# Kernel optimization log

Measured on AMD Instinct MI355X. Metric: run time of the kernel, lower is better.

## Reference

```python
import jax, jax.numpy as jnp
import numpy as np

TGT, BSZ, E, H, HD, P = 256, 64, 1024, 16, 64, 16
TAU = 3.0  # gumbel temperature
SCALE = 1.0 / np.sqrt(HD)


def setup_inputs() -> dict:
    rng = jax.random.key(0)
    ks = jax.random.split(rng, 14)
    n = lambda i, s: jax.random.normal(ks[i], s, dtype=jnp.float32)
    u = jax.random.uniform(ks[7], (BSZ, 2), dtype=jnp.float32, minval=1e-6, maxval=1.0 - 1e-6)
    return {
        'idx': 0,
        'query': n(0, (TGT, BSZ, E)),
        'key': n(1, (TGT, BSZ, E)),
        'value': n(2, (TGT, BSZ, E)),
        'prefix': n(3, (BSZ, 2, P, E)) * 0.5,  # gathered prefix_pool[prompt_ids]
        'batch_weight': jax.random.uniform(ks[4], (BSZ,), dtype=jnp.float32),
        'ori_image_features': n(5, (BSZ, 512)),
        'gumbel_noise': -jnp.log(-jnp.log(u)),  # standard gumbel(0,1) noise
        'in_proj_w': n(8, (3 * E, E)) * 0.02,
        'in_proj_b': jnp.zeros((3 * E,), jnp.float32),
        'out_w': n(9, (E, E)) * 0.02,
        'out_b': jnp.zeros((E,), jnp.float32),
        'gumbel_w': n(10, (2, 512)) * 0.05,
        'gumbel_b': jnp.zeros((2,), jnp.float32),
    }


def _sdpa(q, k, v):
    # q:[b,h,t,d] k,v:[b,h,s,d]
    s = jnp.einsum('bhtd,bhsd->bhts', q, k) * SCALE
    a = jax.nn.softmax(s, axis=-1)
    return jnp.einsum('bhts,bhsd->bhtd', a, v)


def reference(idx, query, key, value, prefix, batch_weight, ori_image_features,
              gumbel_noise, in_proj_w, in_proj_b, out_w, out_b, gumbel_w, gumbel_b):
    tgt, bsz, e = query.shape
    src = key.shape[0]
    # packed in-projection (w chunked into q/k/v blocks)
    w_q, w_k, w_v = jnp.split(in_proj_w, 3, axis=0)
    b_q, b_k, b_v = jnp.split(in_proj_b, 3, axis=0)
    q = query @ w_q.T + b_q            # [t,b,E]
    k = key @ w_k.T + b_k              # [s,b,E]
    v = value @ w_v.T + b_v
    # -> [b,h,t,d]
    q = q.reshape(tgt, bsz, H, HD).transpose(1, 2, 0, 3)
    k = k.reshape(src, bsz, H, HD).transpose(1, 2, 0, 3)
    v = v.reshape(src, bsz, H, HD).transpose(1, 2, 0, 3)
    # prefix k/v: [b,P,E] -> [b,h,P,d] (no in-projection, used raw as in source)
    pk = prefix[:, 0].reshape(bsz, P, H, HD).transpose(0, 2, 1, 3)
    pv = prefix[:, 1].reshape(bsz, P, H, HD).transpose(0, 2, 1, 3)

    attn = _sdpa(q, k, v)                      # [b,h,t,d]
    attn_flat = attn.transpose(2, 0, 1, 3).reshape(tgt * bsz, e)  # (t,b) row order

    attn_pre = _sdpa(q, pk, pv) * batch_weight[:, None, None, None]
    attn_pre_flat = attn_pre.transpose(2, 0, 1, 3).reshape(tgt * bsz, e)

    # gumbel-softmax gate (soft), one 2-way gate per sample
    logits = ori_image_features @ gumbel_w.T + gumbel_b           # [b,2]
    gumbel = jax.nn.softmax((logits + gumbel_noise) / TAU, axis=-1)
    gate = jnp.repeat(gumbel, tgt, axis=0)                        # [b*t,2] (b,t) order, as in source
    combined = attn_flat * gate[:, :1] + (attn_flat + attn_pre_flat) * gate[:, 1:2]

    out = combined @ out_w.T + out_b
    return out.reshape(tgt, bsz, e)
```

## Files before the change

### kernel.cpp

```cpp
#include <hip/hip_runtime.h>

typedef __attribute__((ext_vector_type(8))) short bf16x8;
typedef __attribute__((ext_vector_type(4))) float f32x4;
typedef __attribute__((ext_vector_type(8))) unsigned short ushort8;
typedef __attribute__((ext_vector_type(4))) unsigned short ushort4v;
typedef __attribute__((ext_vector_type(4))) float float4v;
typedef __attribute__((ext_vector_type(2))) unsigned int uint2v;
typedef __attribute__((ext_vector_type(4))) unsigned int uint4v;

#define TGT 256
#define BSZ 64
#define EMB 1024
#define NH 16
#define HD 64
#define PP 16

__device__ __forceinline__ float b2f(unsigned short u) {
  return __builtin_bit_cast(float, ((unsigned int)u) << 16);
}
__device__ __forceinline__ unsigned short f2b(float f) {
  unsigned int u = __builtin_bit_cast(unsigned int, f);
  u += 0x7fffu + ((u >> 16) & 1u);
  return (unsigned short)(u >> 16);
}
__device__ __forceinline__ unsigned int pack2(float lo, float hi) {
  return (unsigned int)f2b(lo) | ((unsigned int)f2b(hi) << 16);
}
__device__ __forceinline__ f32x4 mfma16(bf16x8 a, bf16x8 b, f32x4 c) {
  return __builtin_amdgcn_mfma_f32_16x16x32_bf16(a, b, c, 0, 0, 0);
}
__device__ __forceinline__ void gl_lds16(const unsigned short* g, unsigned short* l) {
  __builtin_amdgcn_global_load_lds(
      (const __attribute__((address_space(1))) unsigned int*)g,
      (__attribute__((address_space(3))) unsigned int*)l, 16, 0, 0);
}

__global__ __launch_bounds__(64) void gate_kernel(
    const float* __restrict__ feat, const float* __restrict__ gw,
    const float* __restrict__ gb, const float* __restrict__ noise,
    float* __restrict__ g1) {
  const int b = blockIdx.x, lane = threadIdx.x;
  float a0 = 0.f, a1 = 0.f;
  for (int i = lane; i < 512; i += 64) {
    float f = feat[b * 512 + i];
    a0 += f * gw[i];
    a1 += f * gw[512 + i];
  }
#pragma unroll
  for (int off = 32; off >= 1; off >>= 1) {
    a0 += __shfl_xor(a0, off);
    a1 += __shfl_xor(a1, off);
  }
  if (lane == 0) {
    float l0 = (a0 + gb[0] + noise[b * 2 + 0]) * (1.0f / 3.0f);
    float l1 = (a1 + gb[1] + noise[b * 2 + 1]) * (1.0f / 3.0f);
    float mm = fmaxf(l0, l1);
    float e0 = __expf(l0 - mm), e1 = __expf(l1 - mm);
    g1[b] = e1 / (e0 + e1);
  }
}

__global__ __launch_bounds__(256) void cast_bf16_kernel(
    const float* __restrict__ in, unsigned short* __restrict__ out, int n8) {
  int i = blockIdx.x * blockDim.x + threadIdx.x;
  const int stride = gridDim.x * blockDim.x;
  for (; i < n8; i += stride) {
    const float4v* p = (const float4v*)(in + (size_t)i * 8);
    float4v v0 = p[0], v1 = p[1];
    ushort8 o = {f2b(v0[0]), f2b(v0[1]), f2b(v0[2]), f2b(v0[3]),
                 f2b(v1[0]), f2b(v1[1]), f2b(v1[2]), f2b(v1[3])};
    *(ushort8*)(out + (size_t)i * 8) = o;
  }
}

#define STEP_WAIT(cntstr)                                \
  asm volatile("s_waitcnt " cntstr ::: "memory");        \
  __builtin_amdgcn_sched_barrier(0);                     \
  __builtin_amdgcn_s_barrier();

#define P3_ISSUE(t, P)                                   \
  {                                                      \
    const float* _p = a32p + (size_t)(t) * 32;           \
    ar[P][0] = *(const float4v*)_p;                      \
    ar[P][1] = *(const float4v*)(_p + 4);                \
    ar[P][2] = *(const float4v*)(_p + 131072);           \
    ar[P][3] = *(const float4v*)(_p + 131072 + 4);       \
  }
#define P3_WRITE(P)                                                     \
  {                                                                     \
    float4v* v = ar[P];                                                 \
    uint4v h0 = {pack2(v[0][0], v[0][1]), pack2(v[0][2], v[0][3]),      \
                 pack2(v[1][0], v[1][1]), pack2(v[1][2], v[1][3])};     \
    uint4v h1 = {pack2(v[2][0], v[2][1]), pack2(v[2][2], v[2][3]),      \
                 pack2(v[3][0], v[3][1]), pack2(v[3][2], v[3][3])};     \
    unsigned short* d = &As[P][swA];                                    \
    *(uint4v*)d = h0;                                                   \
    *(uint4v*)(d + 4096) = h1;                                          \
  }
#define B_STAGE_SLOT(s, SL)                              \
  {                                                      \
    int k0s = (s) * 32;                                  \
    unsigned short* d = &Bs[SL][wl];                     \
    gl_lds16(b0p + k0s, d);                              \
    gl_lds16(b1p + k0s, d + 4096);                       \
  }
#define P3_STEP(s, PAR, BS, DO_IA, DO_SB, DO_W)                       \
  {                                                                   \
    const unsigned short* Ab = &As[PAR][0];                           \
    const unsigned short* Bb = &Bs[BS][0];                            \
    bf16x8 af[8], bfr[4];                                             \
    _Pragma("unroll") for (int mi = 0; mi < 8; ++mi)                  \
        af[mi] = *(const bf16x8*)&Ab[aoff + mi * 512];                \
    _Pragma("unroll") for (int ni = 0; ni < 4; ++ni)                  \
        bfr[ni] = *(const bf16x8*)&Bb[boff + ni * 512];               \
    if (DO_IA) P3_ISSUE((s) + 2, PAR);                                \
    if (DO_SB) B_STAGE_SLOT((s) + 3, ((BS) + 3) & 3);                 \
    __builtin_amdgcn_s_setprio(1);                                    \
    _Pragma("unroll") for (int mi = 0; mi < 8; ++mi)                  \
      _Pragma("unroll") for (int ni = 0; ni < 4; ++ni)                \
        acc[mi][ni] = mfma16(af[mi], bfr[ni], acc[mi][ni]);           \
    __builtin_amdgcn_s_setprio(0);                                    \
    if (DO_W) P3_WRITE((PAR) ^ 1);                 \
  }

__global__ __launch_bounds__(512, 2) void proj3_kernel(
    const float* __restrict__ q, const float* __restrict__ kk,
    const float* __restrict__ vv, const unsigned short* __restrict__ W3,
    const float* __restrict__ bias3, unsigned short* __restrict__ C3) {
  constexpr int K = 1024;
  __shared__ __attribute__((aligned(16))) unsigned short As[2][8192];
  __shared__ __attribute__((aligned(16))) unsigned short Bs[4][8192];
  const int pj = blockIdx.y;
  const float* A = (pj == 0) ? q : ((pj == 1) ? kk : vv);
  const unsigned short* W = W3 + (size_t)pj * 1024 * 1024;
  const float* bias = bias3 + pj * 1024;
  unsigned short* Cv = C3 + (size_t)pj * 16384 * 1024;
  const float qsc = (pj == 0) ? 0.125f : 1.0f;

  const int tid = threadIdx.x;
  const int wv = tid >> 6, lane = tid & 63;
  const int l15 = lane & 15, kg = lane >> 4;
  const int bid = blockIdx.x;
  const int cpx = gridDim.x >> 3;
  const int wg = (bid & 7) * cpx + (bid >> 3);
  const int m0 = (wg >> 2) * 256, n0 = (wg & 3) * 256;
  const int wmL = (wv >> 2) * 128, wnL = (wv & 3) * 64;

  const int sr = wv * 16 + (lane >> 2);
  const int sc = ((lane & 3) * 8) ^ (((sr >> 1) & 3) << 3);
  const float* a32p = A + (size_t)(m0 + sr) * K + (lane & 3) * 8;
  const int swA = sr * 32 + (((lane & 3) ^ ((sr >> 1) & 3)) << 3);
  float4v ar[2][4];
  const unsigned short* b0p = W + (size_t)(n0 + sr) * K + sc;
  const unsigned short* b1p = b0p + (size_t)128 * K;
  const int wl = wv * 512;

  const int x = ((l15 >> 1) & 3) << 3;
  const int aoff = (wmL + l15) * 32 + ((kg * 8) ^ x);
  const int boff = (wnL + l15) * 32 + ((kg * 8) ^ x);

  f32x4 acc[8][4];
#pragma unroll
  for (int i = 0; i < 8; ++i)
#pragma unroll
    for (int j = 0; j < 4; ++j) acc[i][j] = (f32x4){0.f, 0.f, 0.f, 0.f};

  P3_ISSUE(0, 0); B_STAGE_SLOT(0, 0); P3_ISSUE(1, 1); B_STAGE_SLOT(1, 1);
  B_STAGE_SLOT(2, 2);
  P3_WRITE(0);
  STEP_WAIT("vmcnt(8) lgkmcnt(0)")

#pragma unroll 1
  for (int sb = 0; sb < 28; sb += 4) {
    P3_STEP(sb + 0, 0, 0, 1, 1, 1);
    STEP_WAIT("vmcnt(8) lgkmcnt(0)")
    P3_STEP(sb + 1, 1, 1, 1, 1, 1);
    STEP_WAIT("vmcnt(8) lgkmcnt(0)")
    P3_STEP(sb + 2, 0, 2, 1, 1, 1);
    STEP_WAIT("vmcnt(8) lgkmcnt(0)")
    P3_STEP(sb + 3, 1, 3, 1, 1, 1);
    STEP_WAIT("vmcnt(8) lgkmcnt(0)")
  }
  P3_STEP(28, 0, 0, 1, 1, 1);
  STEP_WAIT("vmcnt(8) lgkmcnt(0)")
  P3_STEP(29, 1, 1, 1, 0, 1);
  STEP_WAIT("vmcnt(8) lgkmcnt(0)")
  P3_STEP(30, 0, 2, 0, 0, 1);
  STEP_WAIT("vmcnt(0) lgkmcnt(0)")
  P3_STEP(31, 1, 3, 0, 0, 0);

#pragma unroll
  for (int mi = 0; mi < 8; ++mi) {
#pragma unroll
    for (int ni = 0; ni < 4; ++ni) {
      int col = n0 + wnL + ni * 16 + l15;
      float bcol = bias[col];
#pragma unroll
      for (int r = 0; r < 4; ++r) {
        int row = m0 + wmL + mi * 16 + kg * 4 + r;
        float v = (acc[mi][ni][r] + bcol) * qsc;
        int t = row >> 6, bb = row & 63, hh = col >> 6, dd = col & 63;
        Cv[(size_t)((bb * 16 + hh) * 256 + t) * 64 + dd] = f2b(v);
      }
    }
  }
}

#define O_AOFF(s) (((s) >> 1) * 16384 + ((s)&1) * 32)
#define O_STAGE_A(s)                                     \
  {                                                      \
    const unsigned short* _ap = abf + O_AOFF(s);         \
    unsigned short* d = &As[(s) & 3][wl];                \
    gl_lds16(_ap, d);                                    \
    gl_lds16(_ap + 128, d + 4096);                       \
  }
#define O_STAGE_B(s)                                     \
  {                                                      \
    int k0s = (s) * 32;                                  \
    unsigned short* d = &Bs[(s) & 3][wl];                \
    gl_lds16(b0p + k0s, d);                              \
    gl_lds16(b1p + k0s, d + 4096);                       \
  }
#define O_STEP(s, DO_STAGE)                                           \
  {                                                                   \
    const unsigned short* Ab = &As[(s) & 3][0];                       \
    const unsigned short* Bb = &Bs[(s) & 3][0];                       \
    bf16x8 af[8], bfr[4];                                             \
    _Pragma("unroll") for (int mi = 0; mi < 8; ++mi)                  \
        af[mi] = *(const bf16x8*)&Ab[aoff + mi * 512];                \
    _Pragma("unroll") for (int ni = 0; ni < 4; ++ni)                  \
        bfr[ni] = *(const bf16x8*)&Bb[boff + ni * 512];               \
    if (DO_STAGE) {                                                   \
      O_STAGE_A((s) + 3);                                             \
      O_STAGE_B((s) + 3);                                             \
    }                                                                 \
    __builtin_amdgcn_s_setprio(1);                                    \
    _Pragma("unroll") for (int mi = 0; mi < 8; ++mi)                  \
      _Pragma("unroll") for (int ni = 0; ni < 4; ++ni)                \
        acc[mi][ni] = mfma16(af[mi], bfr[ni], acc[mi][ni]);           \
    __builtin_amdgcn_s_setprio(0);                                    \
  }

__global__ __launch_bounds__(512, 2) void gemm256o_kernel(
    const unsigned short* __restrict__ A, const unsigned short* __restrict__ W,
    const float* __restrict__ bias, float* __restrict__ Cv) {
  constexpr int K = 1024, N = 1024;
  __shared__ __attribute__((aligned(16))) unsigned short As[4][8192];
  __shared__ __attribute__((aligned(16))) unsigned short Bs[4][8192];
  const int tid = threadIdx.x;
  const int wv = tid >> 6, lane = tid & 63;
  const int l15 = lane & 15, kg = lane >> 4;
  const int bid = blockIdx.x;
  const int cpx = gridDim.x >> 3;
  const int wg = (bid & 7) * cpx + (bid >> 3);
  const int m0 = (wg >> 2) * 256, n0 = (wg & 3) * 256;
  const int wmL = (wv >> 2) * 128, wnL = (wv & 3) * 64;

  const int sr = wv * 16 + (lane >> 2);
  const int sc = ((lane & 3) * 8) ^ (((sr >> 1) & 3) << 3);
  const int srg = m0 + sr;
  const unsigned short* abf =
      A + (size_t)(srg & 63) * 262144 + (srg >> 6) * 64 + sc;
  const unsigned short* b0p = W + (size_t)(n0 + sr) * K + sc;
  const unsigned short* b1p = b0p + (size_t)128 * K;
  const int wl = wv * 512;

  const int x = ((l15 >> 1) & 3) << 3;
  const int aoff = (wmL + l15) * 32 + ((kg * 8) ^ x);
  const int boff = (wnL + l15) * 32 + ((kg * 8) ^ x);

  f32x4 acc[8][4];
#pragma unroll
  for (int i = 0; i < 8; ++i)
#pragma unroll
    for (int j = 0; j < 4; ++j) acc[i][j] = (f32x4){0.f, 0.f, 0.f, 0.f};

  O_STAGE_A(0); O_STAGE_B(0); O_STAGE_A(1); O_STAGE_B(1); O_STAGE_A(2); O_STAGE_B(2);
  STEP_WAIT("vmcnt(8)")

  for (int s = 0; s < 29; ++s) {
    O_STEP(s, 1);
    STEP_WAIT("vmcnt(8)")
  }
  O_STEP(29, 0);
  STEP_WAIT("vmcnt(4)")
  O_STEP(30, 0);
  STEP_WAIT("vmcnt(0)")
  O_STEP(31, 0);

#pragma unroll
  for (int mi = 0; mi < 8; ++mi) {
#pragma unroll
    for (int ni = 0; ni < 4; ++ni) {
      int col = n0 + wnL + ni * 16 + l15;
      float bcol = bias[col];
#pragma unroll
      for (int r = 0; r < 4; ++r) {
        int row = m0 + wmL + mi * 16 + kg * 4 + r;
        Cv[(size_t)row * N + col] = acc[mi][ni][r] + bcol;
      }
    }
  }
}

__global__ __launch_bounds__(512) void attn_kernel(
    const unsigned short* __restrict__ qb, const unsigned short* __restrict__ kb,
    const unsigned short* __restrict__ vb, const float* __restrict__ prefix,
    const float* __restrict__ bw, const float* __restrict__ g1,
    unsigned short* __restrict__ comb) {
  const int b = blockIdx.x, h = blockIdx.y;
  __shared__ __attribute__((aligned(16))) unsigned short Kl[256][64];
  __shared__ __attribute__((aligned(16))) unsigned short Vt[64 * 256];
  __shared__ __attribute__((aligned(16))) unsigned short PKl[16][64];
  __shared__ __attribute__((aligned(16))) unsigned short PVt[64][32];
  __shared__ __attribute__((aligned(16))) unsigned short Plds[8][16][40];
  unsigned short* Cb = &Kl[0][0];
  const int tid = threadIdx.x;
  const int wv = tid >> 6, lane = tid & 63;
  const size_t slab = (size_t)(b * NH + h) * 16384;

#pragma unroll
  for (int it = 0; it < 4; ++it) {
    int cid = tid + it * 512;
    int j = cid >> 3, c = cid & 7;
    gl_lds16(kb + slab + (size_t)j * 64 + ((c ^ (j & 7)) << 3),
             &Kl[0][0] + (size_t)(it * 512 + wv * 64) * 8);
    ushort8 vv = *(const ushort8*)(vb + slab + (size_t)j * 64 + (c << 3));
#pragma unroll
    for (int i = 0; i < 8; ++i) {
      int gran = (j >> 3) ^ i ^ c;
      Vt[(c * 8 + i) * 256 + gran * 8 + (j & 7)] = vv[i];
    }
  }
  if (tid < 256) {
    int arr = tid >> 7, cid = tid & 127;
    int sp = cid >> 3, c = cid & 7;
    const float* src = prefix + ((size_t)(b * 2 + arr) * PP + sp) * EMB + h * HD + c * 8;
    float4v v0 = *(const float4v*)src;
    float4v v1 = *(const float4v*)(src + 4);
    if (arr == 0) {
      ushort8 o = {f2b(v0[0]), f2b(v0[1]), f2b(v0[2]), f2b(v0[3]),
                   f2b(v1[0]), f2b(v1[1]), f2b(v1[2]), f2b(v1[3])};
      *(ushort8*)&PKl[sp][((c ^ (sp & 7)) << 3)] = o;
    } else {
#pragma unroll
      for (int i = 0; i < 8; ++i)
        PVt[c * 8 + i][sp] = f2b(i < 4 ? v0[i] : v1[i - 4]);
    }
  } else if (tid < 384) {
    int cid = tid - 256;
    *(ushort8*)&PVt[cid >> 1][16 + (cid & 1) * 8] = (ushort8){0, 0, 0, 0, 0, 0, 0, 0};
  }
  __syncthreads();

  const int l15 = lane & 15, g = lane >> 4;
  const int swl = l15 & 7;
  const float bwb = bw[b];
  unsigned short(&Pw)[16][40] = Plds[wv];

  const int t0 = wv * 32 + l15;
  const size_t qbase = slab + (size_t)t0 * 64;
  bf16x8 qf[2][2];
  qf[0][0] = *(const bf16x8*)(qb + qbase + g * 8);
  qf[0][1] = *(const bf16x8*)(qb + qbase + 32 + g * 8);
  qf[1][0] = *(const bf16x8*)(qb + qbase + 1024 + g * 8);
  qf[1][1] = *(const bf16x8*)(qb + qbase + 1024 + 32 + g * 8);

  f32x4 O[2][4];
#pragma unroll
  for (int st = 0; st < 2; ++st)
#pragma unroll
    for (int dt = 0; dt < 4; ++dt) O[st][dt] = (f32x4){0.f, 0.f, 0.f, 0.f};
  float m[2] = {-3.0e38f, -3.0e38f}, l[2] = {0.f, 0.f};

#pragma unroll
  for (int ch = 0; ch < 8; ++ch) {
    const int rA = ch * 32 + l15, rB = rA + 16;
    bf16x8 ka0 = *(const bf16x8*)&Kl[rA][((g ^ swl) << 3)];
    bf16x8 ka1 = *(const bf16x8*)&Kl[rA][(((4 + g) ^ swl) << 3)];
    bf16x8 kb0 = *(const bf16x8*)&Kl[rB][((g ^ swl) << 3)];
    bf16x8 kb1 = *(const bf16x8*)&Kl[rB][(((4 + g) ^ swl) << 3)];
    f32x4 s[2][2];
#pragma unroll
    for (int st = 0; st < 2; ++st) {
      s[st][0] = (f32x4){0.f, 0.f, 0.f, 0.f};
      s[st][1] = (f32x4){0.f, 0.f, 0.f, 0.f};
      s[st][0] = mfma16(ka0, qf[st][0], s[st][0]);
      s[st][0] = mfma16(ka1, qf[st][1], s[st][0]);
      s[st][1] = mfma16(kb0, qf[st][0], s[st][1]);
      s[st][1] = mfma16(kb1, qf[st][1], s[st][1]);
    }
    bf16x8 pf[2];
#pragma unroll
    for (int st = 0; st < 2; ++st) {
      f32x4 sa = s[st][0], sb = s[st][1];
      float mx = fmaxf(fmaxf(fmaxf(sa[0], sa[1]), fmaxf(sa[2], sa[3])),
                       fmaxf(fmaxf(sb[0], sb[1]), fmaxf(sb[2], sb[3])));
      mx = fmaxf(mx, __shfl_xor(mx, 16));
      mx = fmaxf(mx, __shfl_xor(mx, 32));
      if (__ballot(mx > m[st] + 8.0f) != 0ull) {
        float mn = fmaxf(m[st], mx);
        float f = __expf(m[st] - mn);
        m[st] = mn;
        l[st] *= f;
#pragma unroll
        for (int dt = 0; dt < 4; ++dt)
#pragma unroll
          for (int r = 0; r < 4; ++r) O[st][dt][r] *= f;
      }
      float pA[4], pB[4];
#pragma unroll
      for (int r = 0; r < 4; ++r) {
        pA[r] = __expf(sa[r] - m[st]);
        pB[r] = __expf(sb[r] - m[st]);
      }
      uint2v wa = {pack2(pA[0], pA[1]), pack2(pA[2], pA[3])};
      uint2v wb2 = {pack2(pB[0], pB[1]), pack2(pB[2], pB[3])};
      *(uint2v*)&Pw[l15][g * 4] = wa;
      *(uint2v*)&Pw[l15][16 + g * 4] = wb2;
      float sloc = b2f((unsigned short)(wa[0] & 0xffff)) + b2f((unsigned short)(wa[0] >> 16)) +
                   b2f((unsigned short)(wa[1] & 0xffff)) + b2f((unsigned short)(wa[1] >> 16)) +
                   b2f((unsigned short)(wb2[0] & 0xffff)) + b2f((unsigned short)(wb2[0] >> 16)) +
                   b2f((unsigned short)(wb2[1] & 0xffff)) + b2f((unsigned short)(wb2[1] >> 16));
      l[st] += sloc;
      pf[st] = *(const bf16x8*)&Pw[l15][g * 8];
    }
#pragma unroll
    for (int dt = 0; dt < 4; ++dt) {
      const int drow = dt * 16 + l15;
      const int gran = (ch * 4 + g) ^ (drow & 7) ^ (drow >> 3);
      bf16x8 vf = *(const bf16x8*)&Vt[drow * 256 + gran * 8];
      O[0][dt] = mfma16(vf, pf[0], O[0][dt]);
      O[1][dt] = mfma16(vf, pf[1], O[1][dt]);
    }
  }

#pragma unroll
  for (int st = 0; st < 2; ++st) {
    float lf = l[st];
    lf += __shfl_xor(lf, 16);
    lf += __shfl_xor(lf, 32);
    float inv = 1.0f / lf;
#pragma unroll
    for (int dt = 0; dt < 4; ++dt)
#pragma unroll
      for (int r = 0; r < 4; ++r) O[st][dt][r] *= inv;
  }

  {
    bf16x8 pk0 = *(const bf16x8*)&PKl[l15][((g ^ swl) << 3)];
    bf16x8 pk1 = *(const bf16x8*)&PKl[l15][(((4 + g) ^ swl) << 3)];
    bf16x8 ppf[2];
#pragma unroll
    for (int st = 0; st < 2; ++st) {
      f32x4 sp4 = (f32x4){0.f, 0.f, 0.f, 0.f};
      sp4 = mfma16(pk0, qf[st][0], sp4);
      sp4 = mfma16(pk1, qf[st][1], sp4);
      float pm = fmaxf(fmaxf(sp4[0], sp4[1]), fmaxf(sp4[2], sp4[3]));
      pm = fmaxf(pm, __shfl_xor(pm, 16));
      pm = fmaxf(pm, __shfl_xor(pm, 32));
      float pe[4], pl = 0.f;
#pragma unroll
      for (int r = 0; r < 4; ++r) {
        pe[r] = __expf(sp4[r] - pm);
        pl += pe[r];
      }
      pl += __shfl_xor(pl, 16);
      pl += __shfl_xor(pl, 32);
      float cpre = g1[(t0 + 16 * st) >> 2] * bwb / pl;
#pragma unroll
      for (int r = 0; r < 4; ++r) pe[r] *= cpre;
      *(uint2v*)&Pw[l15][g * 4] = (uint2v){pack2(pe[0], pe[1]), pack2(pe[2], pe[3])};
      *(uint2v*)&Pw[l15][16 + g * 4] = (uint2v){0u, 0u};
      ppf[st] = *(const bf16x8*)&Pw[l15][g * 8];
    }
#pragma unroll
    for (int dt = 0; dt < 4; ++dt) {
      bf16x8 pvf = *(const bf16x8*)&PVt[dt * 16 + l15][g * 8];
      O[0][dt] = mfma16(pvf, ppf[0], O[0][dt]);
      O[1][dt] = mfma16(pvf, ppf[1], O[1][dt]);
    }
  }

  __syncthreads();
#pragma unroll
  for (int st = 0; st < 2; ++st) {
    int t = wv * 32 + st * 16 + l15;
#pragma unroll
    for (int dt = 0; dt < 4; ++dt) {
#pragma unroll
      for (int u = 0; u < 2; ++u) {
        unsigned int pw = pack2(O[st][dt][2 * u], O[st][dt][2 * u + 1]);
        int d = dt * 16 + g * 4 + 2 * u;
        *(unsigned int*)&Cb[t * 64 + (((d >> 3) ^ (t & 7)) << 3) + (d & 7)] = pw;
      }
    }
  }
  __syncthreads();
#pragma unroll
  for (int it = 0; it < 4; ++it) {
    int cid = tid + it * 512;
    int j = cid >> 3, c = cid & 7;
    ushort8 row = *(const ushort8*)&Cb[j * 64 + ((c ^ (j & 7)) << 3)];
    *(ushort8*)(comb + slab + (size_t)j * 64 + (c << 3)) = row;
  }
}

extern "C" void kernel_launch(void* const* d_in, const int* in_sizes, int n_in,
                              void* d_out, int out_size, void* d_ws, size_t ws_size,
                              hipStream_t stream) {
  const float* query = (const float*)d_in[1];
  const float* key = (const float*)d_in[2];
  const float* value = (const float*)d_in[3];
  const float* prefix = (const float*)d_in[4];
  const float* bw = (const float*)d_in[5];
  const float* feat = (const float*)d_in[6];
  const float* noise = (const float*)d_in[7];
  const float* ipw = (const float*)d_in[8];
  const float* ipb = (const float*)d_in[9];
  const float* outw = (const float*)d_in[10];
  const float* outb = (const float*)d_in[11];
  const float* gw = (const float*)d_in[12];
  const float* gb = (const float*)d_in[13];
  float* out = (float*)d_out;

  char* ws = (char*)d_ws;
  const size_t MATB = (size_t)16384 * 1024;
  unsigned short* qb = (unsigned short*)ws;
  unsigned short* kb = qb + MATB;
  unsigned short* vb = kb + MATB;
  unsigned short* cb = vb + MATB;
  unsigned short* wip = cb + MATB;
  unsigned short* wo = wip + (size_t)3072 * 1024;
  float* g1 = (float*)(wo + (size_t)1024 * 1024);

  gate_kernel<<<64, 64, 0, stream>>>(feat, gw, gb, noise, g1);

  cast_bf16_kernel<<<1536, 256, 0, stream>>>(ipw, wip, 3072 * 1024 / 8);
  cast_bf16_kernel<<<512, 256, 0, stream>>>(outw, wo, 1024 * 1024 / 8);

  proj3_kernel<<<dim3(256, 3), 512, 0, stream>>>(query, key, value, wip, ipb, qb);

  attn_kernel<<<dim3(64, 16), 512, 0, stream>>>(qb, kb, vb, prefix, bw, g1, cb);

  gemm256o_kernel<<<256, 512, 0, stream>>>(cb, wo, outb, out);
}
```

Before: 264.2 us.

## Prefetch LDS fragments one step ahead and split fused projection into three launches

Both GEMM kernels now double-buffer their register fragments, reading the next k-step's A (and B for the output projection) from LDS while the current MFMAs run. The projection's A buffer in LDS grows from 2 to 4 slots, the fp32 input loads are issued one step earlier, and the query scale becomes a template constant. The single 3-way projection launch is replaced by three separate launches. These changes aim to hide LDS read latency behind the matrix math, but they raise register pressure at two blocks per CU and add launch gaps between the projections.

Measured after the change: 297.0 us. 12.4% more time.

```diff
diff --git a/kernel.cpp b/kernel.cpp
--- a/kernel.cpp
+++ b/kernel.cpp
@@ -78,7 +78,7 @@
   __builtin_amdgcn_sched_barrier(0);                     \
   __builtin_amdgcn_s_barrier();
 
-#define P3_ISSUE(t, P)                                   \
+#define PJ_ISSUE(t, P)                                   \
   {                                                      \
     const float* _p = a32p + (size_t)(t) * 32;           \
     ar[P][0] = *(const float4v*)_p;                      \
@@ -86,57 +86,54 @@
     ar[P][2] = *(const float4v*)(_p + 131072);           \
     ar[P][3] = *(const float4v*)(_p + 131072 + 4);       \
   }
-#define P3_WRITE(P)                                                     \
+#define PJ_WRITE(t, P)                                                  \
   {                                                                     \
     float4v* v = ar[P];                                                 \
     uint4v h0 = {pack2(v[0][0], v[0][1]), pack2(v[0][2], v[0][3]),      \
                  pack2(v[1][0], v[1][1]), pack2(v[1][2], v[1][3])};     \
     uint4v h1 = {pack2(v[2][0], v[2][1]), pack2(v[2][2], v[2][3]),      \
                  pack2(v[3][0], v[3][1]), pack2(v[3][2], v[3][3])};     \
-    unsigned short* d = &As[P][swA];                                    \
+    unsigned short* d = &As[(t) & 3][swA];                              \
     *(uint4v*)d = h0;                                                   \
     *(uint4v*)(d + 4096) = h1;                                          \
   }
-#define B_STAGE_SLOT(s, SL)                              \
+#define PJ_STAGE_B(s, SL)                                \
   {                                                      \
     int k0s = (s) * 32;                                  \
     unsigned short* d = &Bs[SL][wl];                     \
     gl_lds16(b0p + k0s, d);                              \
     gl_lds16(b1p + k0s, d + 4096);                       \
   }
-#define P3_STEP(s, PAR, BS, DO_IA, DO_SB, DO_W)                       \
+#define PJ_PF_A(s, FP)                                                \
   {                                                                   \
-    const unsigned short* Ab = &As[PAR][0];                           \
+    const unsigned short* Ap = &As[(s) & 3][0];                       \
+    _Pragma("unroll") for (int mi = 0; mi < 8; ++mi)                  \
+        af[FP][mi] = *(const bf16x8*)&Ap[aoff + mi * 512];            \
+  }
+#define PJ_STEP(s, FC, BS, RP, DO_IA, DO_SB, DO_W, DO_PF)             \
+  {                                                                   \
     const unsigned short* Bb = &Bs[BS][0];                            \
-    bf16x8 af[8], bfr[4];                                             \
-    _Pragma("unroll") for (int mi = 0; mi < 8; ++mi)                  \
-        af[mi] = *(const bf16x8*)&Ab[aoff + mi * 512];                \
+    bf16x8 bfr[4];                                                    \
     _Pragma("unroll") for (int ni = 0; ni < 4; ++ni)                  \
         bfr[ni] = *(const bf16x8*)&Bb[boff + ni * 512];               \
-    if (DO_IA) P3_ISSUE((s) + 2, PAR);                                \
-    if (DO_SB) B_STAGE_SLOT((s) + 3, ((BS) + 3) & 3);                 \
+    if (DO_IA) PJ_ISSUE((s) + 3, RP);                                 \
+    if (DO_SB) PJ_STAGE_B((s) + 3, ((BS) + 3) & 3);                   \
+    if (DO_PF) PJ_PF_A((s) + 1, (FC) ^ 1);                            \
     __builtin_amdgcn_s_setprio(1);                                    \
     _Pragma("unroll") for (int mi = 0; mi < 8; ++mi)                  \
       _Pragma("unroll") for (int ni = 0; ni < 4; ++ni)                \
-        acc[mi][ni] = mfma16(af[mi], bfr[ni], acc[mi][ni]);           \
+        acc[mi][ni] = mfma16(af[FC][mi], bfr[ni], acc[mi][ni]);       \
     __builtin_amdgcn_s_setprio(0);                                    \
-    if (DO_W) P3_WRITE((PAR) ^ 1);                 \
-  }
-
-__global__ __launch_bounds__(512, 2) void proj3_kernel(
-    const float* __restrict__ q, const float* __restrict__ kk,
-    const float* __restrict__ vv, const unsigned short* __restrict__ W3,
-    const float* __restrict__ bias3, unsigned short* __restrict__ C3) {
+    if (DO_W) PJ_WRITE((s) + 2, (RP) ^ 1);   \
+  }
+
+template <int QSCALE>
+__global__ __launch_bounds__(512, 2) void proj_kernel(
+    const float* __restrict__ A, const unsigned short* __restrict__ W,
+    const float* __restrict__ bias, unsigned short* __restrict__ Cv) {
   constexpr int K = 1024;
-  __shared__ __attribute__((aligned(16))) unsigned short As[2][8192];
+  __shared__ __attribute__((aligned(16))) unsigned short As[4][8192];
   __shared__ __attribute__((aligned(16))) unsigned short Bs[4][8192];
-  const int pj = blockIdx.y;
-  const float* A = (pj == 0) ? q : ((pj == 1) ? kk : vv);
-  const unsigned short* W = W3 + (size_t)pj * 1024 * 1024;
-  const float* bias = bias3 + pj * 1024;
-  unsigned short* Cv = C3 + (size_t)pj * 16384 * 1024;
-  const float qsc = (pj == 0) ? 0.125f : 1.0f;
-
   const int tid = threadIdx.x;
   const int wv = tid >> 6, lane = tid & 63;
   const int l15 = lane & 15, kg = lane >> 4;
@@ -151,6 +148,7 @@
   const float* a32p = A + (size_t)(m0 + sr) * K + (lane & 3) * 8;
   const int swA = sr * 32 + (((lane & 3) ^ ((sr >> 1) & 3)) << 3);
   float4v ar[2][4];
+  bf16x8 af[2][8];
   const unsigned short* b0p = W + (size_t)(n0 + sr) * K + sc;
   const unsigned short* b1p = b0p + (size_t)128 * K;
   const int wl = wv * 512;
@@ -165,29 +163,32 @@
 #pragma unroll
     for (int j = 0; j < 4; ++j) acc[i][j] = (f32x4){0.f, 0.f, 0.f, 0.f};
 
-  P3_ISSUE(0, 0); B_STAGE_SLOT(0, 0); P3_ISSUE(1, 1); B_STAGE_SLOT(1, 1);
-  B_STAGE_SLOT(2, 2);
-  P3_WRITE(0);
+  PJ_ISSUE(0, 0); PJ_STAGE_B(0, 0); PJ_ISSUE(1, 1); PJ_STAGE_B(1, 1);
+  PJ_STAGE_B(2, 2);
+  PJ_WRITE(0, 0);
+  PJ_ISSUE(2, 0);
+  PJ_WRITE(1, 1);
   STEP_WAIT("vmcnt(8) lgkmcnt(0)")
+  PJ_PF_A(0, 0);
 
 #pragma unroll 1
   for (int sb = 0; sb < 28; sb += 4) {
-    P3_STEP(sb + 0, 0, 0, 1, 1, 1);
+    PJ_STEP(sb + 0, 0, 0, 1, 1, 1, 1, 1);
     STEP_WAIT("vmcnt(8) lgkmcnt(0)")
-    P3_STEP(sb + 1, 1, 1, 1, 1, 1);
+    PJ_STEP(sb + 1, 1, 1, 0, 1, 1, 1, 1);
     STEP_WAIT("vmcnt(8) lgkmcnt(0)")
-    P3_STEP(sb + 2, 0, 2, 1, 1, 1);
+    PJ_STEP(sb + 2, 0, 2, 1, 1, 1, 1, 1);
     STEP_WAIT("vmcnt(8) lgkmcnt(0)")
-    P3_STEP(sb + 3, 1, 3, 1, 1, 1);
+    PJ_STEP(sb + 3, 1, 3, 0, 1, 1, 1, 1);
     STEP_WAIT("vmcnt(8) lgkmcnt(0)")
   }
-  P3_STEP(28, 0, 0, 1, 1, 1);
+  PJ_STEP(28, 0, 0, 1, 1, 1, 1, 1);
   STEP_WAIT("vmcnt(8) lgkmcnt(0)")
-  P3_STEP(29, 1, 1, 1, 0, 1);
+  PJ_STEP(29, 1, 1, 0, 0, 0, 1, 1);
   STEP_WAIT("vmcnt(8) lgkmcnt(0)")
-  P3_STEP(30, 0, 2, 0, 0, 1);
+  PJ_STEP(30, 0, 2, 1, 0, 0, 0, 1);
   STEP_WAIT("vmcnt(0) lgkmcnt(0)")
-  P3_STEP(31, 1, 3, 0, 0, 0);
+  PJ_STEP(31, 1, 3, 0, 0, 0, 0, 0);
 
 #pragma unroll
   for (int mi = 0; mi < 8; ++mi) {
@@ -198,7 +199,8 @@
 #pragma unroll
       for (int r = 0; r < 4; ++r) {
         int row = m0 + wmL + mi * 16 + kg * 4 + r;
-        float v = (acc[mi][ni][r] + bcol) * qsc;
+        float v = acc[mi][ni][r] + bcol;
+        if constexpr (QSCALE) v *= 0.125f;
         int t = row >> 6, bb = row & 63, hh = col >> 6, dd = col & 63;
         Cv[(size_t)((bb * 16 + hh) * 256 + t) * 64 + dd] = f2b(v);
       }
@@ -206,42 +208,39 @@
   }
 }
 
-#define O_AOFF(s) (((s) >> 1) * 16384 + ((s)&1) * 32)
-#define O_STAGE_A(s)                                     \
+#define OP_AOFF(s) (((s) >> 1) * 16384 + ((s)&1) * 32)
+#define OP_STAGE(s, SL)                                  \
   {                                                      \
-    const unsigned short* _ap = abf + O_AOFF(s);         \
-    unsigned short* d = &As[(s) & 3][wl];                \
-    gl_lds16(_ap, d);                                    \
-    gl_lds16(_ap + 128, d + 4096);                       \
-  }
-#define O_STAGE_B(s)                                     \
-  {                                                      \
+    const unsigned short* _ap = abf + OP_AOFF(s);        \
+    unsigned short* da = &As[SL][wl];                    \
+    gl_lds16(_ap, da);                                   \
+    gl_lds16(_ap + 128, da + 4096);                      \
     int k0s = (s) * 32;                                  \
-    unsigned short* d = &Bs[(s) & 3][wl];                \
-    gl_lds16(b0p + k0s, d);                              \
-    gl_lds16(b1p + k0s, d + 4096);                       \
-  }
-#define O_STEP(s, DO_STAGE)                                           \
+    unsigned short* db = &Bs[SL][wl];                    \
+    gl_lds16(b0p + k0s, db);                             \
+    gl_lds16(b1p + k0s, db + 4096);                      \
+  }
+#define OP_PF(s, FP)                                                  \
   {                                                                   \
-    const unsigned short* Ab = &As[(s) & 3][0];                       \
-    const unsigned short* Bb = &Bs[(s) & 3][0];                       \
-    bf16x8 af[8], bfr[4];                                             \
+    const unsigned short* Ap = &As[(s) & 3][0];                       \
+    const unsigned short* Bp = &Bs[(s) & 3][0];                       \
     _Pragma("unroll") for (int mi = 0; mi < 8; ++mi)                  \
-        af[mi] = *(const bf16x8*)&Ab[aoff + mi * 512];                \
+        af[FP][mi] = *(const bf16x8*)&Ap[aoff + mi * 512];            \
     _Pragma("unroll") for (int ni = 0; ni < 4; ++ni)                  \
-        bfr[ni] = *(const bf16x8*)&Bb[boff + ni * 512];               \
-    if (DO_STAGE) {                                                   \
-      O_STAGE_A((s) + 3);                                             \
-      O_STAGE_B((s) + 3);                                             \
-    }                                                                 \
+        bfr[FP][ni] = *(const bf16x8*)&Bp[boff + ni * 512];           \
+  }
+#define OP_STEP(s, FC, BS, DO_SG, DO_PF)                              \
+  {                                                                   \
+    if (DO_SG) OP_STAGE((s) + 3, ((BS) + 3) & 3);                     \
+    if (DO_PF) OP_PF((s) + 1, (FC) ^ 1);                              \
     __builtin_amdgcn_s_setprio(1);                                    \
     _Pragma("unroll") for (int mi = 0; mi < 8; ++mi)                  \
       _Pragma("unroll") for (int ni = 0; ni < 4; ++ni)                \
-        acc[mi][ni] = mfma16(af[mi], bfr[ni], acc[mi][ni]);           \
+        acc[mi][ni] = mfma16(af[FC][mi], bfr[FC][ni], acc[mi][ni]);   \
     __builtin_amdgcn_s_setprio(0);                                    \
   }
 
-__global__ __launch_bounds__(512, 2) void gemm256o_kernel(
+__global__ __launch_bounds__(512, 2) void outproj_kernel(
     const unsigned short* __restrict__ A, const unsigned short* __restrict__ W,
     const float* __restrict__ bias, float* __restrict__ Cv) {
   constexpr int K = 1024, N = 1024;
@@ -269,24 +268,35 @@
   const int aoff = (wmL + l15) * 32 + ((kg * 8) ^ x);
   const int boff = (wnL + l15) * 32 + ((kg * 8) ^ x);
 
+  bf16x8 af[2][8], bfr[2][4];
   f32x4 acc[8][4];
 #pragma unroll
   for (int i = 0; i < 8; ++i)
 #pragma unroll
     for (int j = 0; j < 4; ++j) acc[i][j] = (f32x4){0.f, 0.f, 0.f, 0.f};
 
-  O_STAGE_A(0); O_STAGE_B(0); O_STAGE_A(1); O_STAGE_B(1); O_STAGE_A(2); O_STAGE_B(2);
-  STEP_WAIT("vmcnt(8)")
-
-  for (int s = 0; s < 29; ++s) {
-    O_STEP(s, 1);
-    STEP_WAIT("vmcnt(8)")
-  }
-  O_STEP(29, 0);
+  OP_STAGE(0, 0); OP_STAGE(1, 1); OP_STAGE(2, 2);
   STEP_WAIT("vmcnt(4)")
-  O_STEP(30, 0);
+  OP_PF(0, 0);
+
+#pragma unroll 1
+  for (int sb = 0; sb < 28; sb += 4) {
+    OP_STEP(sb + 0, 0, 0, 1, 1);
+    STEP_WAIT("vmcnt(4)")
+    OP_STEP(sb + 1, 1, 1, 1, 1);
+    STEP_WAIT("vmcnt(4)")
+    OP_STEP(sb + 2, 0, 2, 1, 1);
+    STEP_WAIT("vmcnt(4)")
+    OP_STEP(sb + 3, 1, 3, 1, 1);
+    STEP_WAIT("vmcnt(4)")
+  }
+  OP_STEP(28, 0, 0, 1, 1);
+  STEP_WAIT("vmcnt(4)")
+  OP_STEP(29, 1, 1, 0, 1);
   STEP_WAIT("vmcnt(0)")
-  O_STEP(31, 0);
+  OP_STEP(30, 0, 2, 0, 1);
+  STEP_WAIT("vmcnt(0)")
+  OP_STEP(31, 1, 3, 0, 0);
 
 #pragma unroll
   for (int mi = 0; mi < 8; ++mi) {
@@ -539,9 +549,11 @@
   cast_bf16_kernel<<<1536, 256, 0, stream>>>(ipw, wip, 3072 * 1024 / 8);
   cast_bf16_kernel<<<512, 256, 0, stream>>>(outw, wo, 1024 * 1024 / 8);
 
-  proj3_kernel<<<dim3(256, 3), 512, 0, stream>>>(query, key, value, wip, ipb, qb);
+  proj_kernel<1><<<256, 512, 0, stream>>>(query, wip, ipb, qb);
+  proj_kernel<0><<<256, 512, 0, stream>>>(key, wip + (size_t)1024 * 1024, ipb + 1024, kb);
+  proj_kernel<0><<<256, 512, 0, stream>>>(value, wip + (size_t)2048 * 1024, ipb + 2048, vb);
 
   attn_kernel<<<dim3(64, 16), 512, 0, stream>>>(qb, kb, vb, prefix, bw, g1, cb);
 
-  gemm256o_kernel<<<256, 512, 0, stream>>>(cb, wo, outb, out);
-}
+  outproj_kernel<<<256, 512, 0, stream>>>(cb, wo, outb, out);
+}
```
